# Kernel tuning notes

Measured on AMD Instinct MI355X. Metric: run time of the kernel, lower is better.

## Reference

```python
import jax, jax.numpy as jnp
import numpy as np

N_NODES = 10000
N_EDGES = 160000
N_GRAPHS = 16
IN_FEAT = 128
DIMS = [(128, 512), (512, 256), (256, 64), (64, 32)]


def _lin_params(key, fin, fout):
    w = jax.random.normal(key, (fin, fout), jnp.float32) * (1.0 / np.sqrt(fin))
    b = jnp.zeros((fout,), jnp.float32)
    return w, b


def setup_inputs() -> dict:
    key = jax.random.key(0)
    ks = jax.random.split(key, 64)
    inp = {}
    inp['x'] = jax.random.normal(ks[0], (N_NODES, IN_FEAT), jnp.float32)
    inp['edge_index'] = jax.random.randint(ks[1], (2, N_EDGES), 0, N_NODES, jnp.int64 if jax.config.jax_enable_x64 else jnp.int32)
    inp['batch'] = jnp.sort(jax.random.randint(ks[2], (N_NODES,), 0, N_GRAPHS))
    ki = 3
    for li, (fin, fout) in enumerate(DIMS, start=1):
        for nm in ['q', 'k', 'v', 's']:
            w, b = _lin_params(ks[ki], fin, fout); ki += 1
            inp[f'W{nm}{li}'] = w
            inp[f'b{nm}{li}'] = b
    inp['Wg'], inp['bg'] = _lin_params(ks[ki], 32, 1); ki += 1
    inp['Wf'], inp['bf'] = _lin_params(ks[ki], 32, 9)
    return inp


def _segment_softmax(logits, seg, num_segments):
    m = jax.ops.segment_max(logits, seg, num_segments=num_segments)
    e = jnp.exp(logits - m[seg])
    s = jax.ops.segment_sum(e, seg, num_segments=num_segments)
    return e / s[seg]


def _transformer_conv(x, src, dst, Wq, bq, Wk, bk, Wv, bv, Ws, bs):
    # PyG TransformerConv, heads=1: attention over incoming edges per dst node.
    n = x.shape[0]
    q = x @ Wq + bq
    k = x @ Wk + bk
    v = x @ Wv + bv
    d = q.shape[-1]
    logits = jnp.sum(q[dst] * k[src], axis=-1) / jnp.sqrt(jnp.asarray(d, x.dtype))
    alpha = _segment_softmax(logits, dst, n)  # [E]
    agg = jax.ops.segment_sum(alpha[:, None] * v[src], dst, num_segments=n)
    return agg + (x @ Ws + bs)  # root/skip connection


def reference(x, edge_index, batch,
              Wq1, bq1, Wk1, bk1, Wv1, bv1, Ws1, bs1,
              Wq2, bq2, Wk2, bk2, Wv2, bv2, Ws2, bs2,
              Wq3, bq3, Wk3, bk3, Wv3, bv3, Ws3, bs3,
              Wq4, bq4, Wk4, bk4, Wv4, bv4, Ws4, bs4,
              Wg, bg, Wf, bf):
    src, dst = edge_index[0], edge_index[1]
    layers = [
        (Wq1, bq1, Wk1, bk1, Wv1, bv1, Ws1, bs1),
        (Wq2, bq2, Wk2, bk2, Wv2, bv2, Ws2, bs2),
        (Wq3, bq3, Wk3, bk3, Wv3, bv3, Ws3, bs3),
        (Wq4, bq4, Wk4, bk4, Wv4, bv4, Ws4, bs4),
    ]
    h = x
    for p in layers:
        h = jax.nn.elu(_transformer_conv(h, src, dst, *p))
    # GlobalAttention pooling: gate softmax per graph, weighted sum.
    gate = (h @ Wg + bg)[:, 0]  # [N]
    a = _segment_softmax(gate, batch, N_GRAPHS)
    pooled = jax.ops.segment_sum(a[:, None] * h, batch, num_segments=N_GRAPHS)  # [G, 32]
    return pooled @ Wf + bf  # [G, 9]
```

## Files before the change

kernel.cpp:

```cpp
#include <hip/hip_runtime.h>
#include <hip/hip_bf16.h>
#include <math.h>


typedef __bf16 bf16x8 __attribute__((ext_vector_type(8)));
typedef __bf16 bf16x4 __attribute__((ext_vector_type(4)));
typedef __bf16 bf16x2 __attribute__((ext_vector_type(2)));
typedef float f32x4 __attribute__((ext_vector_type(4)));
typedef float f32x2 __attribute__((ext_vector_type(2)));

#define GBM 128
#define GBN 128
#define GBK 64

#if __has_builtin(__builtin_amdgcn_global_load_lds)
#define ASYNC_LDS 1
__device__ __forceinline__ void gload16(const __bf16* g, __bf16* l) {
  __builtin_amdgcn_global_load_lds(
      (const __attribute__((address_space(1))) unsigned int*)g,
      (__attribute__((address_space(3))) unsigned int*)l, 16, 0, 0);
}
#endif

#if __has_builtin(__builtin_amdgcn_fdot2_f32_bf16)
#define HAS_BF16_DOT2 1
#endif

__global__ __launch_bounds__(256) void gemm_mfma_kernel(
    const __bf16* __restrict__ A, const __bf16* __restrict__ Bt,
    const float* __restrict__ bias, __bf16* __restrict__ qkvs,
    int M, int K, int Nc) {
  __shared__ __bf16 As[GBM * 64];
  __shared__ __bf16 Bs[GBN * 64];
  const int tid = threadIdx.x;
  const int wave = tid >> 6;
  const int lane = tid & 63;
  const int quad = lane >> 4;
  const int l16 = lane & 15;
  const int m0 = blockIdx.y * GBM;
  const int n0 = blockIdx.x * GBN;
  const int wm = (wave & 1) * 64;
  const int wn = (wave >> 1) * 64;

  const int r8 = lane >> 3;
  const int sseg = lane & 7;

  f32x4 acc[4][4] = {};

  for (int k0 = 0; k0 < K; k0 += GBK) {
#pragma unroll
    for (int it = 0; it < 4; ++it) {
      const int rbase = wave * 32 + it * 8;
      const int row = rbase + r8;
      const int sw = sseg ^ r8;
      const __bf16* ga = A + (size_t)(m0 + row) * K + k0 + sw * 8;
      const __bf16* gb = Bt + (size_t)(n0 + row) * K + k0 + sw * 8;
#ifdef ASYNC_LDS
      gload16(ga, As + rbase * 64);
      gload16(gb, Bs + rbase * 64);
#else
      *(bf16x8*)(As + row * 64 + sseg * 8) = *(const bf16x8*)ga;
      *(bf16x8*)(Bs + row * 64 + sseg * 8) = *(const bf16x8*)gb;
#endif
    }
    __syncthreads();

#pragma unroll
    for (int ks = 0; ks < 2; ++ks) {
      bf16x8 af[4], bfr[4];
#pragma unroll
      for (int i = 0; i < 4; ++i) {
        const int ra = wm + i * 16 + l16;
        const int rb = wn + i * 16 + l16;
        const int ps = ((ks * 4 + quad) ^ (l16 & 7)) * 8;
        af[i]  = *(const bf16x8*)(As + ra * 64 + ps);
        bfr[i] = *(const bf16x8*)(Bs + rb * 64 + ps);
      }
#pragma unroll
      for (int mi = 0; mi < 4; ++mi)
#pragma unroll
        for (int ni = 0; ni < 4; ++ni)
          acc[mi][ni] = __builtin_amdgcn_mfma_f32_16x16x32_bf16(
              af[mi], bfr[ni], acc[mi][ni], 0, 0, 0);
    }
    __syncthreads();
  }

  float bsv[4];
#pragma unroll
  for (int ni = 0; ni < 4; ++ni) bsv[ni] = bias[n0 + wn + ni * 16 + l16];
#pragma unroll
  for (int mi = 0; mi < 4; ++mi) {
#pragma unroll
    for (int r = 0; r < 4; ++r) {
      int row = m0 + wm + mi * 16 + quad * 4 + r;
      if (row < M) {
        size_t rb = (size_t)row * Nc;
#pragma unroll
        for (int ni = 0; ni < 4; ++ni) {
          int col = n0 + wn + ni * 16 + l16;
          qkvs[rb + col] = (__bf16)(acc[mi][ni][r] + bsv[ni]);
        }
      }
    }
  }
}

__global__ __launch_bounds__(256) void gemm_mfma_elu_kernel(
    const __bf16* __restrict__ A, const __bf16* __restrict__ Bt,
    const float* __restrict__ bias_s, const float* __restrict__ bias_v,
    const int* __restrict__ offs, __bf16* __restrict__ out,
    int M, int K, int Nc) {
  __shared__ __bf16 As[GBM * 64];
  __shared__ __bf16 Bs[GBN * 64];
  const int tid = threadIdx.x;
  const int wave = tid >> 6;
  const int lane = tid & 63;
  const int quad = lane >> 4;
  const int l16 = lane & 15;
  const int m0 = blockIdx.y * GBM;
  const int n0 = blockIdx.x * GBN;
  const int wm = (wave & 1) * 64;
  const int wn = (wave >> 1) * 64;

  const int r8 = lane >> 3;
  const int sseg = lane & 7;

  f32x4 acc[4][4] = {};

  for (int k0 = 0; k0 < K; k0 += GBK) {
#pragma unroll
    for (int it = 0; it < 4; ++it) {
      const int rbase = wave * 32 + it * 8;
      const int row = rbase + r8;
      const int sw = sseg ^ r8;
      const __bf16* ga = A + (size_t)(m0 + row) * K + k0 + sw * 8;
      const __bf16* gb = Bt + (size_t)(n0 + row) * K + k0 + sw * 8;
#ifdef ASYNC_LDS
      gload16(ga, As + rbase * 64);
      gload16(gb, Bs + rbase * 64);
#else
      *(bf16x8*)(As + row * 64 + sseg * 8) = *(const bf16x8*)ga;
      *(bf16x8*)(Bs + row * 64 + sseg * 8) = *(const bf16x8*)gb;
#endif
    }
    __syncthreads();

#pragma unroll
    for (int ks = 0; ks < 2; ++ks) {
      bf16x8 af[4], bfr[4];
#pragma unroll
      for (int i = 0; i < 4; ++i) {
        const int ra = wm + i * 16 + l16;
        const int rb = wn + i * 16 + l16;
        const int ps = ((ks * 4 + quad) ^ (l16 & 7)) * 8;
        af[i]  = *(const bf16x8*)(As + ra * 64 + ps);
        bfr[i] = *(const bf16x8*)(Bs + rb * 64 + ps);
      }
#pragma unroll
      for (int mi = 0; mi < 4; ++mi)
#pragma unroll
        for (int ni = 0; ni < 4; ++ni)
          acc[mi][ni] = __builtin_amdgcn_mfma_f32_16x16x32_bf16(
              af[mi], bfr[ni], acc[mi][ni], 0, 0, 0);
    }
    __syncthreads();
  }

  float bsv[4], bvv[4];
#pragma unroll
  for (int ni = 0; ni < 4; ++ni) {
    const int col = n0 + wn + ni * 16 + l16;
    bsv[ni] = bias_s[col];
    bvv[ni] = bias_v[col];
  }
#pragma unroll
  for (int mi = 0; mi < 4; ++mi) {
#pragma unroll
    for (int r = 0; r < 4; ++r) {
      int row = m0 + wm + mi * 16 + quad * 4 + r;
      if (row < M) {
        const float bm = (offs[row + 1] - offs[row]) > 0 ? 1.f : 0.f;
        size_t rb = (size_t)row * Nc;
#pragma unroll
        for (int ni = 0; ni < 4; ++ni) {
          int col = n0 + wn + ni * 16 + l16;
          float v = acc[mi][ni][r] + bsv[ni] + bm * bvv[ni];
          v = (v > 0.f) ? v : expm1f(v);
          out[rb + col] = (__bf16)v;
        }
      }
    }
  }
}

#define WTOT 860160
#define BTOT 3456
#define XTOT 320000
#define ATOT 16384
#define UBTOT 128
#define B2TOT 131072
__global__ void pack_all_kernel(
    const float* W0q, const float* W0k, const float* W0v, const float* W0s,
    const float* b0q, const float* b0k, const float* b0v, const float* b0s,
    const float* W1q, const float* W1k, const float* W1v, const float* W1s,
    const float* b1q, const float* b1k, const float* b1v, const float* b1s,
    const float* W2q, const float* W2k, const float* W2v, const float* W2s,
    const float* b2q, const float* b2k, const float* b2v, const float* b2s,
    const float* W3q, const float* W3k, const float* W3v, const float* W3s,
    const float* b3q, const float* b3k, const float* b3v, const float* b3s,
    const float* __restrict__ x, __bf16* __restrict__ xb,
    __bf16* __restrict__ Wt, float* __restrict__ bcat,
    const int* __restrict__ dst, int* __restrict__ deg, int E,
    __bf16* __restrict__ Abt, float* __restrict__ biasu,
    __bf16* __restrict__ Bt2) {
  const int t = blockIdx.x * 256 + threadIdx.x;
  if (t < WTOT) {
    int l, local, ksh, fsh;
    if (t < 262144)      { l = 0; local = t;          ksh = 7; fsh = 9; }
    else if (t < 786432) { l = 1; local = t - 262144; ksh = 9; fsh = 8; }
    else if (t < 851968) { l = 2; local = t - 786432; ksh = 8; fsh = 6; }
    else                 { l = 3; local = t - 851968; ksh = 6; fsh = 5; }
    const int K = 1 << ksh, fout = 1 << fsh;
    int c = local >> ksh;
    int kk = local & (K - 1);
    int blk = c >> fsh;
    int j = c & (fout - 1);
    const float* W;
    if (l == 0)      W = blk == 0 ? W0q : blk == 1 ? W0k : blk == 2 ? W0v : W0s;
    else if (l == 1) W = blk == 0 ? W1q : blk == 1 ? W1k : blk == 2 ? W1v : W1s;
    else if (l == 2) W = blk == 0 ? W2q : blk == 1 ? W2k : blk == 2 ? W2v : W2s;
    else             W = blk == 0 ? W3q : blk == 1 ? W3k : blk == 2 ? W3v : W3s;
    Wt[t] = (__bf16)W[((size_t)kk << fsh) + j];
  } else if (t < WTOT + BTOT) {
    int u = t - WTOT;
    int l, local, fsh, boff;
    if (u < 2048)      { l = 0; local = u;        fsh = 9; boff = 0; }
    else if (u < 3072) { l = 1; local = u - 2048; fsh = 8; boff = 2048; }
    else if (u < 3328) { l = 2; local = u - 3072; fsh = 6; boff = 3072; }
    else               { l = 3; local = u - 3328; fsh = 5; boff = 3328; }
    const int fout = 1 << fsh;
    int blk = local >> fsh, j = local & (fout - 1);
    const float* b;
    if (l == 0)      b = blk == 0 ? b0q : blk == 1 ? b0k : blk == 2 ? b0v : b0s;
    else if (l == 1) b = blk == 0 ? b1q : blk == 1 ? b1k : blk == 2 ? b1v : b1s;
    else if (l == 2) b = blk == 0 ? b2q : blk == 1 ? b2k : blk == 2 ? b2v : b2s;
    else             b = blk == 0 ? b3q : blk == 1 ? b3k : blk == 2 ? b3v : b3s;
    bcat[boff + local] = b[j];
  } else if (t < WTOT + BTOT + XTOT) {
    int i = t - (WTOT + BTOT);
    float4 v = ((const float4*)x)[i];
    bf16x4 o;
    o[0] = (__bf16)v.x; o[1] = (__bf16)v.y; o[2] = (__bf16)v.z; o[3] = (__bf16)v.w;
    *(bf16x4*)(xb + (size_t)i * 4) = o;
  } else if (t < WTOT + BTOT + XTOT + E) {
    int e = t - (WTOT + BTOT + XTOT);
    atomicAdd(&deg[dst[e]], 1);
  } else {
    int u2 = t - (WTOT + BTOT + XTOT + E);
    if (u2 < ATOT) {
      const int n = u2 >> 7;
      const int k = u2 & 127;
      const float4* wq = (const float4*)(W0q + (size_t)k * 512);
      const float4* wk = (const float4*)(W0k + (size_t)n * 512);
      float sacc = 0.f;
#pragma unroll 4
      for (int j = 0; j < 128; ++j) {
        float4 a = wq[j], b = wk[j];
        sacc += a.x * b.x + a.y * b.y + a.z * b.z + a.w * b.w;
      }
      Abt[(size_t)n * 128 + k] = (__bf16)sacc;
    } else if (u2 < ATOT + UBTOT) {
      const int n = u2 - ATOT;
      const float4* wk = (const float4*)(W0k + (size_t)n * 512);
      const float4* bq = (const float4*)b0q;
      float sacc = 0.f;
#pragma unroll 4
      for (int j = 0; j < 128; ++j) {
        float4 a = wk[j], b = bq[j];
        sacc += a.x * b.x + a.y * b.y + a.z * b.z + a.w * b.w;
      }
      biasu[n] = sacc;
    } else if (u2 < ATOT + UBTOT + B2TOT) {
      const int i = u2 - (ATOT + UBTOT);
      const int n = i >> 8;
      const int k = i & 255;
      float v = (k < 128) ? W0v[(size_t)k * 512 + n]
                          : W0s[(size_t)(k - 128) * 512 + n];
      Bt2[(size_t)n * 256 + k] = (__bf16)v;
    }
  }
}

__global__ __launch_bounds__(1024) void scan_kernel(const int* __restrict__ deg,
                                                    int* __restrict__ offs, int N) {
  __shared__ int sums[1024];
  const int tid = threadIdx.x;
  const int chunk = (N + 1023) / 1024;
  const int start = tid * chunk;
  int s = 0;
  for (int i = 0; i < chunk; ++i) {
    int idx = start + i;
    if (idx < N) s += deg[idx];
  }
  sums[tid] = s;
  __syncthreads();
  for (int off = 1; off < 1024; off <<= 1) {
    int t = (tid >= off) ? sums[tid - off] : 0;
    __syncthreads();
    sums[tid] += t;
    __syncthreads();
  }
  int run = (tid == 0) ? 0 : sums[tid - 1];
  for (int i = 0; i < chunk; ++i) {
    int idx = start + i;
    if (idx < N) {
      offs[idx] = run;
      run += deg[idx];
    }
  }
  if (tid == 1023) offs[N] = sums[1023];
}

__global__ void scatter_kernel(const int* __restrict__ src, const int* __restrict__ dst,
                               const int* __restrict__ offs, int* __restrict__ cursor,
                               int* __restrict__ csr_src, int E) {
  int e = blockIdx.x * blockDim.x + threadIdx.x;
  if (e >= E) return;
  int d = dst[e];
  int pos = offs[d] + atomicAdd(&cursor[d], 1);
  csr_src[pos] = src[e];
}

template <int D, int LPG_LOG2, bool GATE>
__global__ __launch_bounds__(256) void attn_fused_kernel(
    const __bf16* __restrict__ qkvs, const int* __restrict__ csr_src,
    const int* __restrict__ offs, __bf16* __restrict__ h_out, int N,
    float scale, const float* __restrict__ Wg, const float* __restrict__ bg,
    float* __restrict__ gate_out) {
  constexpr int LPG = 1 << LPG_LOG2;
  constexpr int NG = 64 / LPG;
  constexpr int NIT = D / (8 * LPG);
  constexpr int LD = 4 * D;
  const int node = (blockIdx.x * 256 + threadIdx.x) >> 6;
  const int lane = threadIdx.x & 63;
  if (node >= N) return;
  const int g = lane >> LPG_LOG2;
  const int l = lane & (LPG - 1);
  const int begin = offs[node];
  const int deg = offs[node + 1] - begin;

  const __bf16* qrow = qkvs + (size_t)node * LD;
  bf16x8 qreg[NIT];
#pragma unroll
  for (int it = 0; it < NIT; ++it)
    qreg[it] = *(const bf16x8*)(qrow + it * LPG * 8 + l * 8);

  float m0 = 0.f;
  float s = 0.f;
  f32x2 acc[NIT][4] = {};

  for (int base = 0; base < deg; base += NG) {
    const int i = base + g;
    const bool valid = i < deg;
    const int sidx = valid ? csr_src[begin + i] : 0;
    const __bf16* krow = qkvs + (size_t)sidx * LD + D;
    bf16x8 kv[NIT], vv[NIT];
    if (valid) {
#pragma unroll
      for (int it = 0; it < NIT; ++it) {
        kv[it] = *(const bf16x8*)(krow + it * LPG * 8 + l * 8);
        vv[it] = *(const bf16x8*)(krow + D + it * LPG * 8 + l * 8);
      }
    }
    float p = 0.f;
    if (valid) {
#ifdef HAS_BF16_DOT2
#pragma unroll
      for (int it = 0; it < NIT; ++it)
#pragma unroll
        for (int j2 = 0; j2 < 4; ++j2) {
          bf16x2 qa; qa[0] = qreg[it][2 * j2]; qa[1] = qreg[it][2 * j2 + 1];
          bf16x2 ka; ka[0] = kv[it][2 * j2];   ka[1] = kv[it][2 * j2 + 1];
          p = __builtin_amdgcn_fdot2_f32_bf16(qa, ka, p, false);
        }
#else
#pragma unroll
      for (int it = 0; it < NIT; ++it)
#pragma unroll
        for (int j = 0; j < 8; ++j) p += (float)qreg[it][j] * (float)kv[it][j];
#endif
    }
#pragma unroll
    for (int off = LPG >> 1; off; off >>= 1) p += __shfl_xor(p, off);
    const float logit = valid ? p * scale : -INFINITY;

    if (base == 0) {
      float mm = logit;
#pragma unroll
      for (int off = LPG; off < 64; off <<= 1)
        mm = fmaxf(mm, __shfl_xor(mm, off));
      m0 = mm;
    }

    const float w = __expf(logit - m0);
    s += w;
    if (valid) {
      f32x2 w2; w2[0] = w; w2[1] = w;
#pragma unroll
      for (int it = 0; it < NIT; ++it)
#pragma unroll
        for (int j2 = 0; j2 < 4; ++j2) {
          f32x2 vf;
          vf[0] = (float)vv[it][2 * j2];
          vf[1] = (float)vv[it][2 * j2 + 1];
          acc[it][j2] += w2 * vf;
        }
    }
  }

#pragma unroll
  for (int off = LPG; off < 64; off <<= 1) {
    s += __shfl_xor(s, off);
#pragma unroll
    for (int it = 0; it < NIT; ++it)
#pragma unroll
      for (int j2 = 0; j2 < 4; ++j2) {
        acc[it][j2][0] += __shfl_xor(acc[it][j2][0], off);
        acc[it][j2][1] += __shfl_xor(acc[it][j2][1], off);
      }
  }
  const float inv = (deg > 0) ? (1.0f / s) : 0.f;

  if (g == 0) {
    float rr[NIT][8];
#pragma unroll
    for (int it = 0; it < NIT; ++it) {
      const int f0 = it * LPG * 8 + l * 8;
      bf16x8 sk = *(const bf16x8*)(qrow + 3 * D + f0);
      bf16x8 o;
#pragma unroll
      for (int j2 = 0; j2 < 4; ++j2) {
        float r0 = acc[it][j2][0] * inv + (float)sk[2 * j2];
        float r1 = acc[it][j2][1] * inv + (float)sk[2 * j2 + 1];
        r0 = (r0 > 0.f) ? r0 : expm1f(r0);
        r1 = (r1 > 0.f) ? r1 : expm1f(r1);
        rr[it][2 * j2] = r0;
        rr[it][2 * j2 + 1] = r1;
        o[2 * j2] = (__bf16)r0;
        o[2 * j2 + 1] = (__bf16)r1;
      }
      *(bf16x8*)(h_out + (size_t)node * D + f0) = o;
    }
    if (GATE) {
      float gp = 0.f;
#pragma unroll
      for (int j = 0; j < 8; ++j) gp += rr[0][j] * Wg[l * 8 + j];
#pragma unroll
      for (int off = 1; off < LPG; off <<= 1) gp += __shfl_xor(gp, off);
      if (l == 0) gate_out[node] = gp + bg[0];
    }
  }
}

template <int LPG_LOG2>
__global__ __launch_bounds__(256) void attn_lin_kernel(
    const __bf16* __restrict__ u, const __bf16* __restrict__ hsrc,
    const int* __restrict__ csr_src, const int* __restrict__ offs,
    __bf16* __restrict__ buf, int N, float scale) {
  constexpr int D = 128;
  constexpr int LPG = 1 << LPG_LOG2;
  constexpr int NG = 64 / LPG;
  constexpr int NIT = D / (8 * LPG);
  const int node = (blockIdx.x * 256 + threadIdx.x) >> 6;
  const int lane = threadIdx.x & 63;
  if (node >= N) return;
  const int g = lane >> LPG_LOG2;
  const int l = lane & (LPG - 1);
  const int begin = offs[node];
  const int deg = offs[node + 1] - begin;

  const __bf16* urow = u + (size_t)node * D;
  bf16x8 qreg[NIT];
#pragma unroll
  for (int it = 0; it < NIT; ++it)
    qreg[it] = *(const bf16x8*)(urow + it * LPG * 8 + l * 8);

  float m0 = 0.f;
  float s = 0.f;
  f32x2 acc[NIT][4] = {};

  for (int base = 0; base < deg; base += NG) {
    const int i = base + g;
    const bool valid = i < deg;
    const int sidx = valid ? csr_src[begin + i] : 0;
    const __bf16* hr = hsrc + (size_t)sidx * D;
    bf16x8 kv[NIT];
    if (valid) {
#pragma unroll
      for (int it = 0; it < NIT; ++it)
        kv[it] = *(const bf16x8*)(hr + it * LPG * 8 + l * 8);
    }
    float p = 0.f;
    if (valid) {
#ifdef HAS_BF16_DOT2
#pragma unroll
      for (int it = 0; it < NIT; ++it)
#pragma unroll
        for (int j2 = 0; j2 < 4; ++j2) {
          bf16x2 qa; qa[0] = qreg[it][2 * j2]; qa[1] = qreg[it][2 * j2 + 1];
          bf16x2 ka; ka[0] = kv[it][2 * j2];   ka[1] = kv[it][2 * j2 + 1];
          p = __builtin_amdgcn_fdot2_f32_bf16(qa, ka, p, false);
        }
#else
#pragma unroll
      for (int it = 0; it < NIT; ++it)
#pragma unroll
        for (int j = 0; j < 8; ++j) p += (float)qreg[it][j] * (float)kv[it][j];
#endif
    }
#pragma unroll
    for (int off = LPG >> 1; off; off >>= 1) p += __shfl_xor(p, off);
    const float logit = valid ? p * scale : -INFINITY;

    if (base == 0) {
      float mm = logit;
#pragma unroll
      for (int off = LPG; off < 64; off <<= 1)
        mm = fmaxf(mm, __shfl_xor(mm, off));
      m0 = mm;
    }

    const float w = __expf(logit - m0);
    s += w;
    if (valid) {
      f32x2 w2; w2[0] = w; w2[1] = w;
#pragma unroll
      for (int it = 0; it < NIT; ++it)
#pragma unroll
        for (int j2 = 0; j2 < 4; ++j2) {
          f32x2 vf;
          vf[0] = (float)kv[it][2 * j2];
          vf[1] = (float)kv[it][2 * j2 + 1];
          acc[it][j2] += w2 * vf;
        }
    }
  }

#pragma unroll
  for (int off = LPG; off < 64; off <<= 1) {
    s += __shfl_xor(s, off);
#pragma unroll
    for (int it = 0; it < NIT; ++it)
#pragma unroll
      for (int j2 = 0; j2 < 4; ++j2) {
        acc[it][j2][0] += __shfl_xor(acc[it][j2][0], off);
        acc[it][j2][1] += __shfl_xor(acc[it][j2][1], off);
      }
  }
  const float inv = (deg > 0) ? (1.0f / s) : 0.f;

  if (g == 0) {
#pragma unroll
    for (int it = 0; it < NIT; ++it) {
      const int f0 = it * LPG * 8 + l * 8;
      bf16x8 o;
#pragma unroll
      for (int j2 = 0; j2 < 4; ++j2) {
        o[2 * j2]     = (__bf16)(acc[it][j2][0] * inv);
        o[2 * j2 + 1] = (__bf16)(acc[it][j2][1] * inv);
      }
      *(bf16x8*)(buf + (size_t)node * 256 + f0) = o;
      *(bf16x8*)(buf + (size_t)node * 256 + 128 + f0) =
          *(const bf16x8*)(hsrc + (size_t)node * D + f0);
    }
  }
}

__global__ __launch_bounds__(256) void pool_final_kernel(
    const __bf16* __restrict__ h, const float* __restrict__ gate,
    const int* __restrict__ batch, int N, const float* __restrict__ Wf,
    const float* __restrict__ bf_, float* __restrict__ out) {
  __shared__ float red[256];
  __shared__ float pooled_s[32];
  __shared__ float m_s, inv_s;
  __shared__ int sb[2];
  const int g = blockIdx.x;
  const int tid = threadIdx.x;

  if (tid < 2) {
    int target = g + tid;
    int lo = 0, hi = N;
    while (lo < hi) {
      int mid = (lo + hi) >> 1;
      if (batch[mid] < target) lo = mid + 1;
      else hi = mid;
    }
    sb[tid] = lo;
  }
  __syncthreads();
  const int s = sb[0];
  const int e_end = sb[1];

  float m = -INFINITY;
  for (int i = s + tid; i < e_end; i += 256) m = fmaxf(m, gate[i]);
  red[tid] = m;
  __syncthreads();
  for (int off = 128; off; off >>= 1) {
    if (tid < off) red[tid] = fmaxf(red[tid], red[tid + off]);
    __syncthreads();
  }
  if (tid == 0) m_s = red[0];
  __syncthreads();
  m = m_s;

  float ss = 0.f;
  for (int i = s + tid; i < e_end; i += 256) ss += __expf(gate[i] - m);
  red[tid] = ss;
  __syncthreads();
  for (int off = 128; off; off >>= 1) {
    if (tid < off) red[tid] += red[tid + off];
    __syncthreads();
  }
  if (tid == 0) inv_s = (e_end > s) ? (1.0f / red[0]) : 0.f;
  __syncthreads();
  const float inv = inv_s;

  const int f = tid & 31;
  const int grp = tid >> 5;
  float acc = 0.f;
  for (int i = s + grp; i < e_end; i += 8)
    acc += __expf(gate[i] - m) * (float)h[(size_t)i * 32 + f];
  red[tid] = acc;
  __syncthreads();
  if (tid < 32) {
    float a = 0.f;
#pragma unroll
    for (int j = 0; j < 8; ++j) a += red[j * 32 + tid];
    pooled_s[tid] = a * inv;
  }
  __syncthreads();

  if (tid < 9) {
    float o = bf_[tid];
#pragma unroll
    for (int kk = 0; kk < 32; ++kk) o += pooled_s[kk] * Wf[kk * 9 + tid];
    out[g * 9 + tid] = o;
  }
}

extern "C" void kernel_launch(void* const* d_in, const int* in_sizes, int n_in,
                              void* d_out, int out_size, void* d_ws, size_t ws_size,
                              hipStream_t stream) {
  const int N = in_sizes[2];
  const int E = in_sizes[1] / 2;
  const int G = 16;
  const int NP = N + 128;

  const float* x = (const float*)d_in[0];
  const int* ei = (const int*)d_in[1];
  const int* batch = (const int*)d_in[2];
  const int* src = ei;
  const int* dst = ei + E;
  const float* Wg = (const float*)d_in[35];
  const float* bg = (const float*)d_in[36];
  const float* Wf = (const float*)d_in[37];
  const float* bf_ = (const float*)d_in[38];
  float* out = (float*)d_out;

  char* p = (char*)d_ws;
  auto carve = [&](size_t bytes) -> char* {
    char* r = p;
    p += (bytes + 255) & ~(size_t)255;
    return r;
  };
  int* deg = (int*)carve((size_t)2 * N * 4);
  int* cursor = deg + N;
  int* offs = (int*)carve((size_t)(N + 1) * 4);
  int* csr_src = (int*)carve((size_t)E * 4);
  __bf16* Ab = (__bf16*)carve((size_t)NP * 128 * 2);
  __bf16* Wt = (__bf16*)carve((size_t)WTOT * 2);
  float* bcat = (float*)carve(BTOT * 4);
  __bf16* qkvs = (__bf16*)carve((size_t)NP * 1024 * 2);
  __bf16* ha = (__bf16*)carve((size_t)NP * 512 * 2);
  __bf16* hb = (__bf16*)carve((size_t)NP * 512 * 2);
  float* gate = (float*)carve((size_t)N * 4);
  __bf16* ubuf = (__bf16*)carve((size_t)NP * 128 * 2);
  __bf16* cat = (__bf16*)carve((size_t)NP * 256 * 2);
  __bf16* Abt = (__bf16*)carve((size_t)ATOT * 2);
  float* biasu = (float*)carve((size_t)UBTOT * 4);
  __bf16* Bt2 = (__bf16*)carve((size_t)B2TOT * 2);
  (void)ws_size;

  hipMemsetAsync(deg, 0, (size_t)2 * N * 4, stream);
  const float** di = (const float**)d_in;
  pack_all_kernel<<<(WTOT + BTOT + XTOT + E + ATOT + UBTOT + B2TOT + 255) / 256,
                    256, 0, stream>>>(
      di[3], di[5], di[7], di[9], di[4], di[6], di[8], di[10],
      di[11], di[13], di[15], di[17], di[12], di[14], di[16], di[18],
      di[19], di[21], di[23], di[25], di[20], di[22], di[24], di[26],
      di[27], di[29], di[31], di[33], di[28], di[30], di[32], di[34],
      x, Ab, Wt, bcat, dst, deg, E, Abt, biasu, Bt2);
  scan_kernel<<<1, 1024, 0, stream>>>(deg, offs, N);
  scatter_kernel<<<(E + 255) / 256, 256, 0, stream>>>(src, dst, offs, cursor, csr_src, E);

  const int agrid = ((size_t)N * 64 + 255) / 256;
  const int mg = (N + GBM - 1) / GBM;

  {
    dim3 g1(1, mg);
    gemm_mfma_kernel<<<g1, 256, 0, stream>>>(Ab, Abt, biasu, ubuf, N, 128, 128);
    attn_lin_kernel<3><<<agrid, 256, 0, stream>>>(ubuf, Ab, csr_src, offs, cat, N,
                                                  1.0f / sqrtf(512.f));
    dim3 g2(4, mg);
    gemm_mfma_elu_kernel<<<g2, 256, 0, stream>>>(cat, Bt2, di[10], di[8], offs,
                                                 ha, N, 256, 512);
  }

  const int fins[3] = {512, 256, 64};
  const int fouts[3] = {256, 64, 32};
  const size_t woffs[3] = {262144, 786432, 851968};
  const int boffs[3] = {2048, 3072, 3328};
  const __bf16* hin = ha;
  __bf16* houts[3] = {hb, ha, hb};

  for (int l = 0; l < 3; ++l) {
    const int fin = fins[l], fout = fouts[l];
    const int Nc = 4 * fout;
    __bf16* hout = houts[l];

    dim3 grid(Nc / GBN, mg);
    gemm_mfma_kernel<<<grid, 256, 0, stream>>>(hin, Wt + woffs[l], bcat + boffs[l],
                                               qkvs, N, fin, Nc);

    float scale = 1.0f / sqrtf((float)fout);
    if (l == 0) {
      attn_fused_kernel<256, 4, false><<<agrid, 256, 0, stream>>>(
          qkvs, csr_src, offs, hout, N, scale, nullptr, nullptr, nullptr);
    } else if (l == 1) {
      attn_fused_kernel<64, 3, false><<<agrid, 256, 0, stream>>>(
          qkvs, csr_src, offs, hout, N, scale, nullptr, nullptr, nullptr);
    } else {
      attn_fused_kernel<32, 2, true><<<agrid, 256, 0, stream>>>(
          qkvs, csr_src, offs, hout, N, scale, Wg, bg, gate);
    }
    hin = hout;
  }

  pool_final_kernel<<<G, 256, 0, stream>>>(hin, gate, batch, N, Wf, bf_, out);
}
```

Measured before the change: 341.6 us.

## Split weight packing into LDS-tiled transpose kernel and parallelize W0q·W0k dot products

The monolithic pack kernel is split in two. A new kernel transposes the layer 1-3 weights and the layer-0 V/S weights through a padded 64x65 shared-memory tile, so both the fp32 reads and the bf16 writes are coalesced instead of strided. It also stops packing the unused layer-0 Q/K/V/S block of Wt. In the remaining kernel, the 128-length Abt and biasu dot products are split across 4 lanes and combined with shuffles, cutting per-thread serial latency at the cost of one extra kernel launch.

```diff
diff --git a/kernel.cpp b/kernel.cpp
--- a/kernel.cpp
+++ b/kernel.cpp
@@ -194,46 +194,85 @@
   }
 }
 
-#define WTOT 860160
+#define NTILES 180
+__global__ __launch_bounds__(256) void transpose_w_kernel(
+    const float* W1q, const float* W1k, const float* W1v, const float* W1s,
+    const float* W2q, const float* W2k, const float* W2v, const float* W2s,
+    const float* W3q, const float* W3k, const float* W3v, const float* W3s,
+    const float* W0v, const float* W0s,
+    __bf16* __restrict__ Wt, __bf16* __restrict__ Bt2) {
+  __shared__ float tile[64][65];
+  const int tb = blockIdx.x;
+  const int tid = threadIdx.x;
+
+  const float* src;
+  __bf16* dst;
+  int K, F, RS, CO, k0, j0;
+  if (tb < 128) {
+    const int m = tb >> 5, t = tb & 31;
+    const float* Ws[4] = {W1q, W1k, W1v, W1s};
+    src = Ws[m]; K = 512; F = 256; RS = 512; CO = 0;
+    k0 = (t & 7) * 64; j0 = (t >> 3) * 64;
+    dst = Wt + 262144 + (size_t)m * 131072;
+  } else if (tb < 144) {
+    const int u = tb - 128, m = u >> 2;
+    const float* Ws[4] = {W2q, W2k, W2v, W2s};
+    src = Ws[m]; K = 256; F = 64; RS = 256; CO = 0;
+    k0 = (u & 3) * 64; j0 = 0;
+    dst = Wt + 786432 + (size_t)m * 16384;
+  } else if (tb < 148) {
+    const int m = tb - 144;
+    const float* Ws[4] = {W3q, W3k, W3v, W3s};
+    src = Ws[m]; K = 64; F = 32; RS = 64; CO = 0;
+    k0 = 0; j0 = 0;
+    dst = Wt + 851968 + (size_t)m * 2048;
+  } else {
+    const int u = tb - 148, m = u >> 4, t = u & 15;
+    src = m ? W0s : W0v; K = 128; F = 512; RS = 256; CO = m * 128;
+    k0 = (t & 1) * 64; j0 = (t >> 1) * 64;
+    dst = Bt2;
+  }
+
+  const int lj = tid & 63;
+  const int lr = tid >> 6;
+#pragma unroll
+  for (int it = 0; it < 16; ++it) {
+    const int kr = it * 4 + lr;
+    float v = 0.f;
+    if (k0 + kr < K && j0 + lj < F) v = src[(size_t)(k0 + kr) * F + j0 + lj];
+    tile[kr][lj] = v;
+  }
+  __syncthreads();
+#pragma unroll
+  for (int it = 0; it < 16; ++it) {
+    const int jr = it * 4 + lr;
+    if (j0 + jr < F && k0 + lj < K)
+      dst[(size_t)(j0 + jr) * RS + CO + k0 + lj] = (__bf16)tile[lj][jr];
+  }
+}
+
 #define BTOT 3456
 #define XTOT 320000
-#define ATOT 16384
-#define UBTOT 128
-#define B2TOT 131072
-__global__ void pack_all_kernel(
-    const float* W0q, const float* W0k, const float* W0v, const float* W0s,
+#define ABT_T 65536
+#define UB_T 512
+__global__ void pack_misc_kernel(
     const float* b0q, const float* b0k, const float* b0v, const float* b0s,
-    const float* W1q, const float* W1k, const float* W1v, const float* W1s,
     const float* b1q, const float* b1k, const float* b1v, const float* b1s,
-    const float* W2q, const float* W2k, const float* W2v, const float* W2s,
     const float* b2q, const float* b2k, const float* b2v, const float* b2s,
-    const float* W3q, const float* W3k, const float* W3v, const float* W3s,
     const float* b3q, const float* b3k, const float* b3v, const float* b3s,
+    const float* W0q, const float* W0k,
     const float* __restrict__ x, __bf16* __restrict__ xb,
-    __bf16* __restrict__ Wt, float* __restrict__ bcat,
+    float* __restrict__ bcat,
     const int* __restrict__ dst, int* __restrict__ deg, int E,
-    __bf16* __restrict__ Abt, float* __restrict__ biasu,
-    __bf16* __restrict__ Bt2) {
+    __bf16* __restrict__ Abt, float* __restrict__ biasu) {
   const int t = blockIdx.x * 256 + threadIdx.x;
-  if (t < WTOT) {
-    int l, local, ksh, fsh;
-    if (t < 262144)      { l = 0; local = t;          ksh = 7; fsh = 9; }
-    else if (t < 786432) { l = 1; local = t - 262144; ksh = 9; fsh = 8; }
-    else if (t < 851968) { l = 2; local = t - 786432; ksh = 8; fsh = 6; }
-    else                 { l = 3; local = t - 851968; ksh = 6; fsh = 5; }
-    const int K = 1 << ksh, fout = 1 << fsh;
-    int c = local >> ksh;
-    int kk = local & (K - 1);
-    int blk = c >> fsh;
-    int j = c & (fout - 1);
-    const float* W;
-    if (l == 0)      W = blk == 0 ? W0q : blk == 1 ? W0k : blk == 2 ? W0v : W0s;
-    else if (l == 1) W = blk == 0 ? W1q : blk == 1 ? W1k : blk == 2 ? W1v : W1s;
-    else if (l == 2) W = blk == 0 ? W2q : blk == 1 ? W2k : blk == 2 ? W2v : W2s;
-    else             W = blk == 0 ? W3q : blk == 1 ? W3k : blk == 2 ? W3v : W3s;
-    Wt[t] = (__bf16)W[((size_t)kk << fsh) + j];
-  } else if (t < WTOT + BTOT) {
-    int u = t - WTOT;
+  if (t < XTOT) {
+    float4 v = ((const float4*)x)[t];
+    bf16x4 o;
+    o[0] = (__bf16)v.x; o[1] = (__bf16)v.y; o[2] = (__bf16)v.z; o[3] = (__bf16)v.w;
+    *(bf16x4*)(xb + (size_t)t * 4) = o;
+  } else if (t < XTOT + BTOT) {
+    int u = t - XTOT;
     int l, local, fsh, boff;
     if (u < 2048)      { l = 0; local = u;        fsh = 9; boff = 0; }
     else if (u < 3072) { l = 1; local = u - 2048; fsh = 8; boff = 2048; }
@@ -247,48 +286,41 @@
     else if (l == 2) b = blk == 0 ? b2q : blk == 1 ? b2k : blk == 2 ? b2v : b2s;
     else             b = blk == 0 ? b3q : blk == 1 ? b3k : blk == 2 ? b3v : b3s;
     bcat[boff + local] = b[j];
-  } else if (t < WTOT + BTOT + XTOT) {
-    int i = t - (WTOT + BTOT);
-    float4 v = ((const float4*)x)[i];
-    bf16x4 o;
-    o[0] = (__bf16)v.x; o[1] = (__bf16)v.y; o[2] = (__bf16)v.z; o[3] = (__bf16)v.w;
-    *(bf16x4*)(xb + (size_t)i * 4) = o;
-  } else if (t < WTOT + BTOT + XTOT + E) {
-    int e = t - (WTOT + BTOT + XTOT);
+  } else if (t < XTOT + BTOT + E) {
+    int e = t - (XTOT + BTOT);
     atomicAdd(&deg[dst[e]], 1);
-  } else {
-    int u2 = t - (WTOT + BTOT + XTOT + E);
-    if (u2 < ATOT) {
-      const int n = u2 >> 7;
-      const int k = u2 & 127;
-      const float4* wq = (const float4*)(W0q + (size_t)k * 512);
-      const float4* wk = (const float4*)(W0k + (size_t)n * 512);
-      float sacc = 0.f;
+  } else if (t < XTOT + BTOT + E + ABT_T) {
+    const int u = t - (XTOT + BTOT + E);
+    const int n = u >> 9;
+    const int rem = u & 511;
+    const int k = rem >> 2;
+    const int q = rem & 3;
+    const float4* wq = (const float4*)(W0q + (size_t)k * 512) + q * 32;
+    const float4* wk = (const float4*)(W0k + (size_t)n * 512) + q * 32;
+    float sacc = 0.f;
 #pragma unroll 4
-      for (int j = 0; j < 128; ++j) {
-        float4 a = wq[j], b = wk[j];
-        sacc += a.x * b.x + a.y * b.y + a.z * b.z + a.w * b.w;
-      }
-      Abt[(size_t)n * 128 + k] = (__bf16)sacc;
-    } else if (u2 < ATOT + UBTOT) {
-      const int n = u2 - ATOT;
-      const float4* wk = (const float4*)(W0k + (size_t)n * 512);
-      const float4* bq = (const float4*)b0q;
-      float sacc = 0.f;
+    for (int jj = 0; jj < 32; ++jj) {
+      float4 a = wq[jj], b = wk[jj];
+      sacc += a.x * b.x + a.y * b.y + a.z * b.z + a.w * b.w;
+    }
+    sacc += __shfl_xor(sacc, 1);
+    sacc += __shfl_xor(sacc, 2);
+    if (q == 0) Abt[(size_t)n * 128 + k] = (__bf16)sacc;
+  } else if (t < XTOT + BTOT + E + ABT_T + UB_T) {
+    const int u = t - (XTOT + BTOT + E + ABT_T);
+    const int n = u >> 2;
+    const int q = u & 3;
+    const float4* wk = (const float4*)(W0k + (size_t)n * 512) + q * 32;
+    const float4* bq = (const float4*)b0q + q * 32;
+    float sacc = 0.f;
 #pragma unroll 4
-      for (int j = 0; j < 128; ++j) {
-        float4 a = wk[j], b = bq[j];
-        sacc += a.x * b.x + a.y * b.y + a.z * b.z + a.w * b.w;
-      }
-      biasu[n] = sacc;
-    } else if (u2 < ATOT + UBTOT + B2TOT) {
-      const int i = u2 - (ATOT + UBTOT);
-      const int n = i >> 8;
-      const int k = i & 255;
-      float v = (k < 128) ? W0v[(size_t)k * 512 + n]
-                          : W0s[(size_t)(k - 128) * 512 + n];
-      Bt2[(size_t)n * 256 + k] = (__bf16)v;
-    }
+    for (int jj = 0; jj < 32; ++jj) {
+      float4 a = wk[jj], b = bq[jj];
+      sacc += a.x * b.x + a.y * b.y + a.z * b.z + a.w * b.w;
+    }
+    sacc += __shfl_xor(sacc, 1);
+    sacc += __shfl_xor(sacc, 2);
+    if (q == 0) biasu[n] = sacc;
   }
 }
 
@@ -649,6 +681,10 @@
   }
 }
 
+#define WTOT 860160
+#define ATOT 16384
+#define UBTOT 128
+#define B2TOT 131072
 extern "C" void kernel_launch(void* const* d_in, const int* in_sizes, int n_in,
                               void* d_out, int out_size, void* d_ws, size_t ws_size,
                               hipStream_t stream) {
@@ -694,13 +730,19 @@
 
   hipMemsetAsync(deg, 0, (size_t)2 * N * 4, stream);
   const float** di = (const float**)d_in;
-  pack_all_kernel<<<(WTOT + BTOT + XTOT + E + ATOT + UBTOT + B2TOT + 255) / 256,
-                    256, 0, stream>>>(
-      di[3], di[5], di[7], di[9], di[4], di[6], di[8], di[10],
-      di[11], di[13], di[15], di[17], di[12], di[14], di[16], di[18],
-      di[19], di[21], di[23], di[25], di[20], di[22], di[24], di[26],
-      di[27], di[29], di[31], di[33], di[28], di[30], di[32], di[34],
-      x, Ab, Wt, bcat, dst, deg, E, Abt, biasu, Bt2);
+  transpose_w_kernel<<<NTILES, 256, 0, stream>>>(
+      di[11], di[13], di[15], di[17],
+      di[19], di[21], di[23], di[25],
+      di[27], di[29], di[31], di[33],
+      di[7], di[9],
+      Wt, Bt2);
+  pack_misc_kernel<<<(XTOT + BTOT + E + ABT_T + UB_T + 255) / 256, 256, 0, stream>>>(
+      di[4], di[6], di[8], di[10],
+      di[12], di[14], di[16], di[18],
+      di[20], di[22], di[24], di[26],
+      di[28], di[30], di[32], di[34],
+      di[3], di[5],
+      x, Ab, bcat, dst, deg, E, Abt, biasu);
   scan_kernel<<<1, 1024, 0, stream>>>(deg, offs, N);
   scatter_kernel<<<(E + 255) / 256, 256, 0, stream>>>(src, dst, offs, cursor, csr_src, E);
 
```

New measurement: 334.3 us. 2.1% less time.
